# Performance work log

Measured on AMD Instinct MI355X. Metric: run time of the kernel, lower is better.

Reference implementation:

```python
import jax, jax.numpy as jnp
import numpy as np

NODES, NFEAT = 128, 256


def setup_inputs() -> dict:
    key = jax.random.key(0)
    k1, k2, k3, k4, k5, k6 = jax.random.split(key, 6)
    B = 512
    x = jax.random.normal(k1, (B, NODES, NFEAT), dtype=jnp.float32)
    adj = jax.random.uniform(k2, (B, NODES, NODES), dtype=jnp.float32)
    # GraphConvolution(nfeat, nfeat): weight [nfeat, nfeat], bias [nfeat]
    s = 1.0 / np.sqrt(NFEAT)
    gcn_w = jax.random.uniform(k3, (NFEAT, NFEAT), minval=-s, maxval=s, dtype=jnp.float32)
    gcn_b = jax.random.uniform(k4, (NFEAT,), minval=-s, maxval=s, dtype=jnp.float32)
    # fc: Linear(nfeat*nodes, nfeat), torch layout [out, in]
    s2 = 1.0 / np.sqrt(NFEAT * NODES)
    fc_w = jax.random.uniform(k5, (NFEAT, NFEAT * NODES), minval=-s2, maxval=s2, dtype=jnp.float32)
    fc_b = jax.random.uniform(k6, (NFEAT,), minval=-s2, maxval=s2, dtype=jnp.float32)
    return {"x": x, "adj": adj, "gcn_w": gcn_w, "gcn_b": gcn_b, "fc_w": fc_w, "fc_b": fc_b}


def reference(x, adj, gcn_w, gcn_b, fc_w, fc_b):
    B = x.shape[0]
    # Per-sample loop GCN fused as batched matmuls:
    # support = X @ W ; out = A @ support + b
    support = jnp.einsum('bnf,fg->bng', x, gcn_w)          # [B, nodes, nfeat]
    mid = jnp.einsum('bnm,bmg->bng', adj, support) + gcn_b  # [B, nodes, nfeat]
    # cat along dim0 then reshape(-1, nfeat*nodes) == per-graph flatten
    flat = mid.reshape(B, NODES * NFEAT)
    output = flat @ fc_w.T + fc_b                           # [B, nfeat]
    useful_input = x[:, 0, :]                               # [B, nfeat]
    return (output, useful_input, output)
```

## Files before the change

kernel.cpp:

```cpp
#include <hip/hip_runtime.h>

#define NODES 128
#define NFEAT 256
#define BATCH 512
#define KTOT  (NODES * NFEAT)
#define SPLIT 64
#define KCH   (KTOT / SPLIT)

typedef __bf16 bf16_t;
typedef bf16_t bf16x4 __attribute__((ext_vector_type(4)));
typedef bf16_t bf16x8 __attribute__((ext_vector_type(8)));
typedef float  f32x4  __attribute__((ext_vector_type(4)));

#define BK    32
#define LDK   40
#define BK2   64
#define LDK2  72
#define TILE  128

__device__ __forceinline__ void bar() {
    asm volatile("s_waitcnt lgkmcnt(0)\n\ts_barrier" ::: "memory");
}

__device__ __forceinline__ bf16x8 cvt8(const float4 a, const float4 b) {
    bf16x8 t;
    t[0] = (bf16_t)a.x; t[1] = (bf16_t)a.y; t[2] = (bf16_t)a.z; t[3] = (bf16_t)a.w;
    t[4] = (bf16_t)b.x; t[5] = (bf16_t)b.y; t[6] = (bf16_t)b.z; t[7] = (bf16_t)b.w;
    return t;
}

struct XT { float4 v[4]; };
__device__ __forceinline__ void xload(const float* __restrict__ src, int ld, int k0,
                                      int tid, XT& t) {
#pragma unroll
    for (int i = 0; i < 2; i++) {
        int f = tid + i * 256, r = f >> 2, c = f & 3;
        t.v[2 * i]     = *(const float4*)(src + (size_t)r * ld + k0 + c * 8);
        t.v[2 * i + 1] = *(const float4*)(src + (size_t)r * ld + k0 + c * 8 + 4);
    }
}
__device__ __forceinline__ void xstore(bf16_t* __restrict__ dst, int tid, const XT& t) {
#pragma unroll
    for (int i = 0; i < 2; i++) {
        int f = tid + i * 256, r = f >> 2, c = f & 3;
        *(bf16x8*)(dst + r * LDK + c * 8) = cvt8(t.v[2 * i], t.v[2 * i + 1]);
    }
}

struct XT2 { float4 v[8]; };
__device__ __forceinline__ void xload2(const float* __restrict__ src, int ld, int k0,
                                       int tid, XT2& t) {
#pragma unroll
    for (int i = 0; i < 4; i++) {
        int f = tid + i * 256, r = f >> 3, c = f & 7;
        t.v[2 * i]     = *(const float4*)(src + (size_t)r * ld + k0 + c * 8);
        t.v[2 * i + 1] = *(const float4*)(src + (size_t)r * ld + k0 + c * 8 + 4);
    }
}
__device__ __forceinline__ void xstore2(bf16_t* __restrict__ dst, int tid, const XT2& t) {
#pragma unroll
    for (int i = 0; i < 4; i++) {
        int f = tid + i * 256, r = f >> 3, c = f & 7;
        *(bf16x8*)(dst + r * LDK2 + c * 8) = cvt8(t.v[2 * i], t.v[2 * i + 1]);
    }
}

struct AT2 { bf16x8 v[4]; };
__device__ __forceinline__ void aload2(const bf16_t* __restrict__ src, int ld, int k0,
                                       int tid, AT2& t) {
#pragma unroll
    for (int i = 0; i < 4; i++) {
        int f = tid + i * 256, r = f >> 3, c = f & 7;
        t.v[i] = *(const bf16x8*)(src + (size_t)r * ld + k0 + c * 8);
    }
}
__device__ __forceinline__ void astore2(bf16_t* __restrict__ dst, int tid, const AT2& t) {
#pragma unroll
    for (int i = 0; i < 4; i++) {
        int f = tid + i * 256, r = f >> 3, c = f & 7;
        *(bf16x8*)(dst + r * LDK2 + c * 8) = t.v[i];
    }
}

__global__ __launch_bounds__(256)
void k_wt(const float* __restrict__ w, bf16_t* __restrict__ wT) {
    const int g0 = blockIdx.x * 4;
    const int k  = threadIdx.x;
    const float4 v = *(const float4*)(w + (size_t)k * NFEAT + g0);
    wT[(size_t)(g0 + 0) * NFEAT + k] = (bf16_t)v.x;
    wT[(size_t)(g0 + 1) * NFEAT + k] = (bf16_t)v.y;
    wT[(size_t)(g0 + 2) * NFEAT + k] = (bf16_t)v.z;
    wT[(size_t)(g0 + 3) * NFEAT + k] = (bf16_t)v.w;
}

__global__ __launch_bounds__(256, 3)
void k_fused12(const float* __restrict__ x, const float* __restrict__ adj,
               const bf16_t* __restrict__ wT, const float* __restrict__ gcn_b,
               bf16_t* __restrict__ mid) {
    __shared__ __align__(16) bf16_t As[2][TILE * LDK];
    __shared__ __align__(16) bf16_t Sb[TILE * TILE];
    const int n0  = blockIdx.x * TILE;
    const int b   = blockIdx.y;
    const int tid = threadIdx.x;
    const int lane = tid & 63, w = tid >> 6, wm = w & 1, wn = w >> 1;
    const int l15 = lane & 15, q = lane >> 4;
    const float* xb   = x   + (size_t)b * NODES * NFEAT;
    const float* adjb = adj + (size_t)b * NODES * NODES;

    const bf16_t* wrow[4];
#pragma unroll
    for (int j = 0; j < 4; j++)
        wrow[j] = wT + (size_t)(n0 + wn * 64 + j * 16 + l15) * NFEAT + q * 8;

    f32x4 acc[4][4] = {};
    {
        XT r[3];
        xload(xb, NFEAT, 0 * BK, tid, r[0]);
        xload(xb, NFEAT, 1 * BK, tid, r[1]);
        xload(xb, NFEAT, 2 * BK, tid, r[2]);
        xstore(As[0], tid, r[0]);
        bar();
#pragma unroll
        for (int k = 0; k < 8; k++) {
            if (k + 3 < 8) xload(xb, NFEAT, (k + 3) * BK, tid, r[k % 3]);
            bf16x8 bcur[4];
#pragma unroll
            for (int j = 0; j < 4; j++) bcur[j] = *(const bf16x8*)(wrow[j] + k * BK);
            bf16x8 a[4];
#pragma unroll
            for (int i = 0; i < 4; i++)
                a[i] = *(const bf16x8*)(&As[k & 1][(wm * 64 + i * 16 + l15) * LDK + q * 8]);
#pragma unroll
            for (int i = 0; i < 4; i++)
#pragma unroll
                for (int j = 0; j < 4; j++)
                    acc[i][j] = __builtin_amdgcn_mfma_f32_16x16x32_bf16(a[i], bcur[j], acc[i][j], 0, 0, 0);
            if (k + 1 < 8) xstore(As[(k + 1) & 1], tid, r[(k + 1) % 3]);
            bar();
        }
    }

    XT r[3];
    xload(adjb, NODES, 0 * BK, tid, r[0]);
    xload(adjb, NODES, 1 * BK, tid, r[1]);
    xload(adjb, NODES, 2 * BK, tid, r[2]);
#pragma unroll
    for (int i = 0; i < 4; i++)
#pragma unroll
        for (int j = 0; j < 4; j++)
#pragma unroll
            for (int rr = 0; rr < 4; rr++) {
                int m = wm * 64 + i * 16 + q * 4 + rr;
                int g = wn * 64 + j * 16 + l15;
                int slot = (m >> 3) ^ (g & 15);
                Sb[g * 128 + slot * 8 + (m & 7)] = (bf16_t)acc[i][j][rr];
            }
    bar();
    xstore(As[0], tid, r[0]);
    bar();

    f32x4 acc2[4][4] = {};
#pragma unroll
    for (int k = 0; k < 4; k++) {
        if (k + 3 < 4) xload(adjb, NODES, (k + 3) * BK, tid, r[k % 3]);
        bf16x8 a[4], bb[4];
#pragma unroll
        for (int i = 0; i < 4; i++)
            a[i] = *(const bf16x8*)(&As[k & 1][(wm * 64 + i * 16 + l15) * LDK + q * 8]);
#pragma unroll
        for (int j = 0; j < 4; j++) {
            int R = wn * 64 + j * 16 + l15;
            int slot = (k * 4 + q) ^ (R & 15);
            bb[j] = *(const bf16x8*)(&Sb[R * 128 + slot * 8]);
        }
#pragma unroll
        for (int i = 0; i < 4; i++)
#pragma unroll
            for (int j = 0; j < 4; j++)
                acc2[i][j] = __builtin_amdgcn_mfma_f32_16x16x32_bf16(a[i], bb[j], acc2[i][j], 0, 0, 0);
        if (k + 1 < 4) xstore(As[(k + 1) & 1], tid, r[(k + 1) % 3]);
        bar();
    }
    bf16_t* outb = mid + (size_t)b * NODES * NFEAT;
#pragma unroll
    for (int j = 0; j < 4; j++) {
        int g = n0 + wn * 64 + j * 16 + l15;
        float bias = gcn_b[g];
#pragma unroll
        for (int i = 0; i < 4; i++)
#pragma unroll
            for (int rr = 0; rr < 4; rr++) {
                int node = wm * 64 + i * 16 + q * 4 + rr;
                outb[(size_t)node * NFEAT + g] = (bf16_t)(acc2[i][j][rr] + bias);
            }
    }
}

__global__ __launch_bounds__(256, 2)
void k_out(const bf16_t* __restrict__ flat, const float* __restrict__ fcw,
           bf16_t* __restrict__ part) {
    __shared__ __align__(16) bf16_t As[2][TILE * LDK2];
    __shared__ __align__(16) bf16_t Bs[2][TILE * LDK2];
    const int m0 = blockIdx.x * TILE;
    const int n0 = blockIdx.y * TILE;
    const int kb = blockIdx.z * KCH;
    const int tid = threadIdx.x;
    const int lane = tid & 63, w = tid >> 6, wm = w & 1, wn = w >> 1;
    const int l15 = lane & 15, q = lane >> 4;
    f32x4 acc[4][4] = {};
    const bf16_t* fa = flat + (size_t)m0 * KTOT;
    const float*  fb = fcw + (size_t)n0 * KTOT;

    AT2 ra[3]; XT2 rb[2];
    aload2(fa, KTOT, kb + 0 * BK2, tid, ra[0]);
    xload2(fb, KTOT, kb + 0 * BK2, tid, rb[0]);
    aload2(fa, KTOT, kb + 1 * BK2, tid, ra[1]);
    xload2(fb, KTOT, kb + 1 * BK2, tid, rb[1]);
    aload2(fa, KTOT, kb + 2 * BK2, tid, ra[2]);
    astore2(As[0], tid, ra[0]);
    xstore2(Bs[0], tid, rb[0]);
    bar();
#pragma unroll
    for (int k = 0; k < 8; k++) {
        if (k + 3 < 8) aload2(fa, KTOT, kb + (k + 3) * BK2, tid, ra[k % 3]);
        if (k + 2 < 8) xload2(fb, KTOT, kb + (k + 2) * BK2, tid, rb[k & 1]);
#pragma unroll
        for (int kk = 0; kk < BK2; kk += BK) {
            bf16x8 a[4], bbf[4];
#pragma unroll
            for (int i = 0; i < 4; i++)
                a[i] = *(const bf16x8*)(&As[k & 1][(wm * 64 + i * 16 + l15) * LDK2 + kk + q * 8]);
#pragma unroll
            for (int j = 0; j < 4; j++)
                bbf[j] = *(const bf16x8*)(&Bs[k & 1][(wn * 64 + j * 16 + l15) * LDK2 + kk + q * 8]);
#pragma unroll
            for (int i = 0; i < 4; i++)
#pragma unroll
                for (int j = 0; j < 4; j++)
                    acc[i][j] = __builtin_amdgcn_mfma_f32_16x16x32_bf16(a[i], bbf[j], acc[i][j], 0, 0, 0);
        }
        if (k + 1 < 8) {
            astore2(As[(k + 1) & 1], tid, ra[(k + 1) % 3]);
            xstore2(Bs[(k + 1) & 1], tid, rb[(k + 1) & 1]);
        }
        bar();
    }
    bf16_t* pb = part + (size_t)blockIdx.z * BATCH * NFEAT;
#pragma unroll
    for (int i = 0; i < 4; i++)
#pragma unroll
        for (int j = 0; j < 4; j++)
#pragma unroll
            for (int r = 0; r < 4; r++) {
                int bt_ = m0 + wm * 64 + i * 16 + q * 4 + r;
                int o   = n0 + wn * 64 + j * 16 + l15;
                pb[(size_t)bt_ * NFEAT + o] = (bf16_t)acc[i][j][r];
            }
}

__global__ __launch_bounds__(256)
void k_reduce(const bf16_t* __restrict__ part, const float* __restrict__ fc_b,
              const float* __restrict__ x, float* __restrict__ out) {
    const int g4 = (blockIdx.x * 256 + threadIdx.x) * 4;
    const int o = g4 & (NFEAT - 1), b = g4 >> 8;
    float s[4];
    const float4 c0 = *(const float4*)(fc_b + o);
    s[0] = c0.x; s[1] = c0.y; s[2] = c0.z; s[3] = c0.w;
#pragma unroll 8
    for (int i = 0; i < SPLIT; i++) {
        bf16x4 p = *(const bf16x4*)(part + (size_t)i * BATCH * NFEAT + g4);
#pragma unroll
        for (int j = 0; j < 4; j++) s[j] += (float)p[j];
    }
    float4 o0 = make_float4(s[0], s[1], s[2], s[3]);
    *(float4*)(out + g4) = o0;
    *(float4*)(out + 2 * BATCH * NFEAT + g4) = o0;
    *(float4*)(out + BATCH * NFEAT + g4) = *(const float4*)(x + (size_t)b * NODES * NFEAT + o);
}

extern "C" void kernel_launch(void* const* d_in, const int* in_sizes, int n_in,
                              void* d_out, int out_size, void* d_ws, size_t ws_size,
                              hipStream_t stream) {
    const float* x     = (const float*)d_in[0];
    const float* adj   = (const float*)d_in[1];
    const float* gcn_w = (const float*)d_in[2];
    const float* gcn_b = (const float*)d_in[3];
    const float* fc_w  = (const float*)d_in[4];
    const float* fc_b  = (const float*)d_in[5];
    float* out = (float*)d_out;

    bf16_t* wT   = (bf16_t*)d_ws;
    bf16_t* mid  = (bf16_t*)((char*)d_ws + 131072);
    bf16_t* part = (bf16_t*)((char*)d_ws + 131072 + (size_t)BATCH * NODES * NFEAT * 2);

    k_wt     <<<dim3(64), dim3(256), 0, stream>>>(gcn_w, wT);
    k_fused12<<<dim3(2, BATCH), dim3(256), 0, stream>>>(x, adj, wT, gcn_b, mid);
    k_out    <<<dim3(4, 2, SPLIT), dim3(256), 0, stream>>>(mid, fc_w, part);
    k_reduce <<<dim3(128), dim3(256), 0, stream>>>(part, fc_b, x, out);
}
```

Baseline: 199.9 us.

## Narrow GCN tile with XCD-aware remap and pre-convert fc weight to bf16

The fused GCN kernel now uses a 64-column output tile, giving 4 blocks per graph and higher occupancy. Its block ids are remapped so that blocks sharing a graph land on the same XCD for L2 reuse. Separately, fc_w is converted to bf16 once per call in a new kernel, and a bf16-input output GEMM reads it, cutting the fp32 weight traffic and the conversion inside the GEMM. The trade-offs are an extra pass over the 32MB fp32 weight, more workspace, and recomputing the X@W product twice as often per graph.

```diff
diff --git a/kernel.cpp b/kernel.cpp
--- a/kernel.cpp
+++ b/kernel.cpp
@@ -17,6 +17,7 @@
 #define BK2   64
 #define LDK2  72
 #define TILE  128
+#define GT    64
 
 __device__ __forceinline__ void bar() {
     asm volatile("s_waitcnt lgkmcnt(0)\n\ts_barrier" ::: "memory");
@@ -93,26 +94,36 @@
     wT[(size_t)(g0 + 3) * NFEAT + k] = (bf16_t)v.w;
 }
 
-__global__ __launch_bounds__(256, 3)
+__global__ __launch_bounds__(256)
+void k_fwt(const float* __restrict__ w, bf16_t* __restrict__ wb) {
+    const size_t i = ((size_t)blockIdx.x * 256 + threadIdx.x) * 8;
+    const float4 a = *(const float4*)(w + i);
+    const float4 b = *(const float4*)(w + i + 4);
+    *(bf16x8*)(wb + i) = cvt8(a, b);
+}
+
+__global__ __launch_bounds__(256, 4)
 void k_fused12(const float* __restrict__ x, const float* __restrict__ adj,
                const bf16_t* __restrict__ wT, const float* __restrict__ gcn_b,
                bf16_t* __restrict__ mid) {
     __shared__ __align__(16) bf16_t As[2][TILE * LDK];
-    __shared__ __align__(16) bf16_t Sb[TILE * TILE];
-    const int n0  = blockIdx.x * TILE;
-    const int b   = blockIdx.y;
+    __shared__ __align__(16) bf16_t Sb[GT * 128];
+    const int id  = blockIdx.y * 4 + blockIdx.x;
+    const int xcd = id & 7, jj = id >> 3;
+    const int b   = (xcd << 6) | (jj >> 2);
+    const int n0  = (jj & 3) * GT;
     const int tid = threadIdx.x;
     const int lane = tid & 63, w = tid >> 6, wm = w & 1, wn = w >> 1;
     const int l15 = lane & 15, q = lane >> 4;
     const float* xb   = x   + (size_t)b * NODES * NFEAT;
     const float* adjb = adj + (size_t)b * NODES * NODES;
 
-    const bf16_t* wrow[4];
-#pragma unroll
-    for (int j = 0; j < 4; j++)
-        wrow[j] = wT + (size_t)(n0 + wn * 64 + j * 16 + l15) * NFEAT + q * 8;
-
-    f32x4 acc[4][4] = {};
+    const bf16_t* wrow[2];
+#pragma unroll
+    for (int j = 0; j < 2; j++)
+        wrow[j] = wT + (size_t)(n0 + wn * 32 + j * 16 + l15) * NFEAT + q * 8;
+
+    f32x4 acc[4][2] = {};
     {
         XT r[3];
         xload(xb, NFEAT, 0 * BK, tid, r[0]);
@@ -123,9 +134,9 @@
 #pragma unroll
         for (int k = 0; k < 8; k++) {
             if (k + 3 < 8) xload(xb, NFEAT, (k + 3) * BK, tid, r[k % 3]);
-            bf16x8 bcur[4];
-#pragma unroll
-            for (int j = 0; j < 4; j++) bcur[j] = *(const bf16x8*)(wrow[j] + k * BK);
+            bf16x8 bcur[2];
+#pragma unroll
+            for (int j = 0; j < 2; j++) bcur[j] = *(const bf16x8*)(wrow[j] + k * BK);
             bf16x8 a[4];
 #pragma unroll
             for (int i = 0; i < 4; i++)
@@ -133,7 +144,7 @@
 #pragma unroll
             for (int i = 0; i < 4; i++)
 #pragma unroll
-                for (int j = 0; j < 4; j++)
+                for (int j = 0; j < 2; j++)
                     acc[i][j] = __builtin_amdgcn_mfma_f32_16x16x32_bf16(a[i], bcur[j], acc[i][j], 0, 0, 0);
             if (k + 1 < 8) xstore(As[(k + 1) & 1], tid, r[(k + 1) % 3]);
             bar();
@@ -147,11 +158,11 @@
 #pragma unroll
     for (int i = 0; i < 4; i++)
 #pragma unroll
-        for (int j = 0; j < 4; j++)
+        for (int j = 0; j < 2; j++)
 #pragma unroll
             for (int rr = 0; rr < 4; rr++) {
                 int m = wm * 64 + i * 16 + q * 4 + rr;
-                int g = wn * 64 + j * 16 + l15;
+                int g = wn * 32 + j * 16 + l15;
                 int slot = (m >> 3) ^ (g & 15);
                 Sb[g * 128 + slot * 8 + (m & 7)] = (bf16_t)acc[i][j][rr];
             }
@@ -159,32 +170,32 @@
     xstore(As[0], tid, r[0]);
     bar();
 
-    f32x4 acc2[4][4] = {};
+    f32x4 acc2[4][2] = {};
 #pragma unroll
     for (int k = 0; k < 4; k++) {
         if (k + 3 < 4) xload(adjb, NODES, (k + 3) * BK, tid, r[k % 3]);
-        bf16x8 a[4], bb[4];
+        bf16x8 a[4], bb[2];
 #pragma unroll
         for (int i = 0; i < 4; i++)
             a[i] = *(const bf16x8*)(&As[k & 1][(wm * 64 + i * 16 + l15) * LDK + q * 8]);
 #pragma unroll
-        for (int j = 0; j < 4; j++) {
-            int R = wn * 64 + j * 16 + l15;
+        for (int j = 0; j < 2; j++) {
+            int R = wn * 32 + j * 16 + l15;
             int slot = (k * 4 + q) ^ (R & 15);
             bb[j] = *(const bf16x8*)(&Sb[R * 128 + slot * 8]);
         }
 #pragma unroll
         for (int i = 0; i < 4; i++)
 #pragma unroll
-            for (int j = 0; j < 4; j++)
+            for (int j = 0; j < 2; j++)
                 acc2[i][j] = __builtin_amdgcn_mfma_f32_16x16x32_bf16(a[i], bb[j], acc2[i][j], 0, 0, 0);
         if (k + 1 < 4) xstore(As[(k + 1) & 1], tid, r[(k + 1) % 3]);
         bar();
     }
     bf16_t* outb = mid + (size_t)b * NODES * NFEAT;
 #pragma unroll
-    for (int j = 0; j < 4; j++) {
-        int g = n0 + wn * 64 + j * 16 + l15;
+    for (int j = 0; j < 2; j++) {
+        int g = n0 + wn * 32 + j * 16 + l15;
         float bias = gcn_b[g];
 #pragma unroll
         for (int i = 0; i < 4; i++)
@@ -194,6 +205,68 @@
                 outb[(size_t)node * NFEAT + g] = (bf16_t)(acc2[i][j][rr] + bias);
             }
     }
+}
+
+__global__ __launch_bounds__(256, 2)
+void k_out_bf(const bf16_t* __restrict__ flat, const bf16_t* __restrict__ fcwb,
+              bf16_t* __restrict__ part) {
+    __shared__ __align__(16) bf16_t As[2][TILE * LDK2];
+    __shared__ __align__(16) bf16_t Bs[2][TILE * LDK2];
+    const int m0 = blockIdx.x * TILE;
+    const int n0 = blockIdx.y * TILE;
+    const int kb = blockIdx.z * KCH;
+    const int tid = threadIdx.x;
+    const int lane = tid & 63, w = tid >> 6, wm = w & 1, wn = w >> 1;
+    const int l15 = lane & 15, q = lane >> 4;
+    f32x4 acc[4][4] = {};
+    const bf16_t* fa = flat + (size_t)m0 * KTOT;
+    const bf16_t* fb = fcwb + (size_t)n0 * KTOT;
+
+    AT2 ra[3], rb[2];
+    aload2(fa, KTOT, kb + 0 * BK2, tid, ra[0]);
+    aload2(fb, KTOT, kb + 0 * BK2, tid, rb[0]);
+    aload2(fa, KTOT, kb + 1 * BK2, tid, ra[1]);
+    aload2(fb, KTOT, kb + 1 * BK2, tid, rb[1]);
+    aload2(fa, KTOT, kb + 2 * BK2, tid, ra[2]);
+    astore2(As[0], tid, ra[0]);
+    astore2(Bs[0], tid, rb[0]);
+    bar();
+#pragma unroll
+    for (int k = 0; k < 8; k++) {
+        if (k + 3 < 8) aload2(fa, KTOT, kb + (k + 3) * BK2, tid, ra[k % 3]);
+        if (k + 2 < 8) aload2(fb, KTOT, kb + (k + 2) * BK2, tid, rb[k & 1]);
+#pragma unroll
+        for (int kk = 0; kk < BK2; kk += BK) {
+            bf16x8 a[4], bbf[4];
+#pragma unroll
+            for (int i = 0; i < 4; i++)
+                a[i] = *(const bf16x8*)(&As[k & 1][(wm * 64 + i * 16 + l15) * LDK2 + kk + q * 8]);
+#pragma unroll
+            for (int j = 0; j < 4; j++)
+                bbf[j] = *(const bf16x8*)(&Bs[k & 1][(wn * 64 + j * 16 + l15) * LDK2 + kk + q * 8]);
+#pragma unroll
+            for (int i = 0; i < 4; i++)
+#pragma unroll
+                for (int j = 0; j < 4; j++)
+                    acc[i][j] = __builtin_amdgcn_mfma_f32_16x16x32_bf16(a[i], bbf[j], acc[i][j], 0, 0, 0);
+        }
+        if (k + 1 < 8) {
+            astore2(As[(k + 1) & 1], tid, ra[(k + 1) % 3]);
+            astore2(Bs[(k + 1) & 1], tid, rb[(k + 1) & 1]);
+        }
+        bar();
+    }
+    bf16_t* pb = part + (size_t)blockIdx.z * BATCH * NFEAT;
+#pragma unroll
+    for (int i = 0; i < 4; i++)
+#pragma unroll
+        for (int j = 0; j < 4; j++)
+#pragma unroll
+            for (int r = 0; r < 4; r++) {
+                int bt_ = m0 + wm * 64 + i * 16 + q * 4 + r;
+                int o   = n0 + wn * 64 + j * 16 + l15;
+                pb[(size_t)bt_ * NFEAT + o] = (bf16_t)acc[i][j][r];
+            }
 }
 
 __global__ __launch_bounds__(256, 2)
@@ -289,12 +362,22 @@
     const float* fc_b  = (const float*)d_in[5];
     float* out = (float*)d_out;
 
+    const size_t midB  = (size_t)BATCH * NODES * NFEAT * 2;
+    const size_t partB = (size_t)SPLIT * BATCH * NFEAT * 2;
+    const size_t fcwB  = (size_t)NFEAT * KTOT * 2;
     bf16_t* wT   = (bf16_t*)d_ws;
     bf16_t* mid  = (bf16_t*)((char*)d_ws + 131072);
-    bf16_t* part = (bf16_t*)((char*)d_ws + 131072 + (size_t)BATCH * NODES * NFEAT * 2);
+    bf16_t* part = (bf16_t*)((char*)d_ws + 131072 + midB);
+    bf16_t* fcwb = (bf16_t*)((char*)d_ws + 131072 + midB + partB);
+    const bool cv = ws_size >= 131072 + midB + partB + fcwB;
 
     k_wt     <<<dim3(64), dim3(256), 0, stream>>>(gcn_w, wT);
-    k_fused12<<<dim3(2, BATCH), dim3(256), 0, stream>>>(x, adj, wT, gcn_b, mid);
-    k_out    <<<dim3(4, 2, SPLIT), dim3(256), 0, stream>>>(mid, fc_w, part);
+    if (cv)
+        k_fwt<<<dim3(4096), dim3(256), 0, stream>>>(fc_w, fcwb);
+    k_fused12<<<dim3(4, BATCH), dim3(256), 0, stream>>>(x, adj, wT, gcn_b, mid);
+    if (cv)
+        k_out_bf<<<dim3(4, 2, SPLIT), dim3(256), 0, stream>>>(mid, fcwb, part);
+    else
+        k_out   <<<dim3(4, 2, SPLIT), dim3(256), 0, stream>>>(mid, fc_w, part);
     k_reduce <<<dim3(128), dim3(256), 0, stream>>>(part, fc_b, x, out);
 }
```

Result: slower. 213.1 us (+6.6%).
